# Kernel optimization log

Hardware: AMD Instinct MI355X
Metric: run time of the kernel (lower is better)

The kernel has to match this reference:

```python
import jax, jax.numpy as jnp
import numpy as np

NUM_CONTROL_POINTS = 4
# Standard Catmull-Rom spline basis (rows map [1, t, t^2, t^3] monomials to control points)
CATMULL_ROM_BASIS = 0.5 * np.array(
    [[0.0, 2.0, 0.0, 0.0],
     [-1.0, 0.0, 1.0, 0.0],
     [2.0, -5.0, 4.0, -1.0],
     [-1.0, 3.0, -3.0, 1.0]], dtype=np.float32)

BATCH, IN_F, OUT_F = 1024, 512, 512


def setup_inputs() -> dict:
    key = jax.random.key(0)
    k1, k2, k3, k4 = jax.random.split(key, 4)
    inp = jax.random.normal(k1, (BATCH, IN_F), dtype=jnp.float32)
    # phase spans [0, 2*pi) so both spline segments (mask = phase < 1.5*pi) are exercised
    phase = jax.random.uniform(k2, (BATCH,), dtype=jnp.float32) * (2.0 * jnp.pi)
    bound = 1.0 / np.sqrt(IN_F)
    weights = jax.random.uniform(k3, (NUM_CONTROL_POINTS, OUT_F, IN_F), dtype=jnp.float32,
                                 minval=-bound, maxval=bound)
    biases = jax.random.uniform(k4, (NUM_CONTROL_POINTS, OUT_F), dtype=jnp.float32,
                                minval=-bound, maxval=bound)
    return {"input": inp, "phase": phase, "weights": weights, "biases": biases}


def _spline_coeffs(phase):
    # Faithful to the original (including its overwrite bug): tt = [1, t^2, t^3, 0]
    basis = jnp.asarray(CATMULL_ROM_BASIS, dtype=phase.dtype)
    t0 = phase / (1.5 * jnp.pi)
    t1 = (phase - 0.5 * jnp.pi) / (1.5 * jnp.pi)
    ones, zeros = jnp.ones_like(phase), jnp.zeros_like(phase)
    tt0 = jnp.stack([ones, t0 * t0, t0 ** 3, zeros], axis=1)  # (B,4)
    tt1 = jnp.stack([ones, t1 * t1, t1 ** 3, zeros], axis=1)  # (B,4)
    mask = (phase < 1.5 * jnp.pi)[:, None]
    # Selecting per-sample coefficients before the weight contraction is exactly
    # equivalent to where(mask, tt0@B@W, tt1@B@W) since the map is linear in tt.
    return jnp.where(mask, tt0 @ basis, tt1 @ basis)  # (B,4) control-point coeffs


def reference(input, phase, weights, biases):
    c = _spline_coeffs(phase)                       # (B,4)
    # Fused form: apply the 4 shared control-point linear layers, then blend,
    # avoiding the (B,out,in) per-sample weight tensor. Same math as
    # (tt@B@W).reshape(B,out,in) @ input[:,:,None] + b.
    y4 = jnp.einsum('bi,coi->bco', input, weights)  # (B,4,out)
    out = jnp.einsum('bc,bco->bo', c, y4) + c @ biases  # (B,out)
    return out
```

## Files before the change

kernel.cpp:

```cpp
#include <hip/hip_runtime.h>


#define BATCH 1024
#define IN_F  512
#define OUT_F 512

constexpr int BM = 32;
constexpr int BO = 64;
constexpr int BK = 32;
constexpr int KITERS = IN_F / BK;
constexpr int A_ELEMS = BM * BK;
constexpr int TILE_ELEMS = (BM + 4 * BO) * BK;
constexpr int NVEC = TILE_ELEMS / 8;

typedef unsigned short u16;
typedef u16    u16x8  __attribute__((ext_vector_type(8)));
typedef __bf16 bf16x8 __attribute__((ext_vector_type(8)));
typedef float  f32x4  __attribute__((ext_vector_type(4)));

__device__ __forceinline__ u16 f2bits(float f) {
  union { float f; unsigned int u; } v; v.f = f;
  unsigned int u = v.u;
  unsigned int r = u + 0x7fffu + ((u >> 16) & 1u);
  return (u16)(r >> 16);
}

__global__ __launch_bounds__(256)
void PhaseLinear_kernel(const float* __restrict__ inp, const float* __restrict__ ph,
                        const float* __restrict__ wts, const float* __restrict__ bia,
                        float* __restrict__ outp) {
  __shared__ alignas(16) u16 sT[2][TILE_ELEMS];
  __shared__ float sCoef[BM][4];

  const int tid = threadIdx.x;
  const int wv  = tid >> 6;
  const int l   = tid & 63;
  const int o0  = blockIdx.x * BO;
  const int b0  = blockIdx.y * BM;

  if (tid < BM) {
    const float PI = 3.14159265358979323846f;
    float p  = ph[b0 + tid];
    float t  = (p < 1.5f * PI) ? (p / (1.5f * PI)) : ((p - 0.5f * PI) / (1.5f * PI));
    float t2 = t * t, t3 = t2 * t;
    sCoef[tid][0] = t3 - 0.5f * t2;
    sCoef[tid][1] = 1.0f - 2.5f * t3;
    sCoef[tid][2] = 0.5f * t2 + 2.0f * t3;
    sCoef[tid][3] = -0.5f * t3;
  }

  const int nv = (tid < NVEC - 1024) ? 5 : 4;
  const float* src[5];
  int loff[5];
#pragma unroll
  for (int j = 0; j < 5; ++j) {
    int v = tid + j * 256;
    if (v >= NVEC) { src[j] = inp; loff[j] = 0; continue; }
    int e = v * 8;
    loff[j] = e;
    if (e < A_ELEMS) {
      int row = e >> 5, col = e & 31;
      src[j] = inp + (size_t)(b0 + row) * IN_F + col;
    } else {
      int ep = e - A_ELEMS;
      int r = ep >> 5, col = ep & 31;
      int c = r >> 6, oo = r & 63;
      src[j] = wts + ((size_t)c * OUT_F + o0 + oo) * IN_F + col;
    }
  }

  f32x4 regs[5][2];
#pragma unroll
  for (int j = 0; j < 5; ++j)
    if (j < nv) {
      regs[j][0] = *(const f32x4*)(src[j]);
      regs[j][1] = *(const f32x4*)(src[j] + 4);
    }

  f32x4 acc[2][4];
#pragma unroll
  for (int m = 0; m < 2; ++m)
#pragma unroll
    for (int c = 0; c < 4; ++c) acc[m][c] = (f32x4){0.f, 0.f, 0.f, 0.f};

  const int q = l >> 4;
  const int n = l & 15;

  for (int kk = 0; kk < KITERS; ++kk) {
    const int bsel = kk & 1;
    u16* buf = &sT[bsel][0];
#pragma unroll
    for (int j = 0; j < 5; ++j)
      if (j < nv) {
        u16x8 pk;
#pragma unroll
        for (int x = 0; x < 4; ++x) {
          pk[x]     = f2bits(regs[j][0][x]);
          pk[x + 4] = f2bits(regs[j][1][x]);
        }
        *(u16x8*)(buf + loff[j]) = pk;
      }
    if (kk + 1 < KITERS) {
#pragma unroll
      for (int j = 0; j < 5; ++j)
        if (j < nv) {
          regs[j][0] = *(const f32x4*)(src[j] + (kk + 1) * BK);
          regs[j][1] = *(const f32x4*)(src[j] + (kk + 1) * BK + 4);
        }
    }
    __syncthreads();
    const u16* pA = buf;
    const u16* pW = buf + A_ELEMS;
    bf16x8 a0 = *(const bf16x8*)(pA + (n)      * BK + q * 8);
    bf16x8 a1 = *(const bf16x8*)(pA + (n + 16) * BK + q * 8);
#pragma unroll
    for (int c = 0; c < 4; ++c) {
      bf16x8 wf = *(const bf16x8*)(pW + (c * 64 + wv * 16 + n) * BK + q * 8);
      acc[0][c] = __builtin_amdgcn_mfma_f32_16x16x32_bf16(a0, wf, acc[0][c], 0, 0, 0);
      acc[1][c] = __builtin_amdgcn_mfma_f32_16x16x32_bf16(a1, wf, acc[1][c], 0, 0, 0);
    }
  }

  const int o = o0 + wv * 16 + n;
  float bs[4];
#pragma unroll
  for (int c = 0; c < 4; ++c) bs[c] = bia[c * OUT_F + o];

#pragma unroll
  for (int mf = 0; mf < 2; ++mf) {
#pragma unroll
    for (int r = 0; r < 4; ++r) {
      const int bl = mf * 16 + q * 4 + r;
      float v = 0.f;
#pragma unroll
      for (int c = 0; c < 4; ++c)
        v += sCoef[bl][c] * (acc[mf][c][r] + bs[c]);
      outp[(size_t)(b0 + bl) * OUT_F + o] = v;
    }
  }
}

extern "C" void kernel_launch(void* const* d_in, const int* in_sizes, int n_in,
                              void* d_out, int out_size, void* d_ws, size_t ws_size,
                              hipStream_t stream) {
  const float* inp = (const float*)d_in[0];
  const float* ph  = (const float*)d_in[1];
  const float* wts = (const float*)d_in[2];
  const float* bia = (const float*)d_in[3];
  float* outp = (float*)d_out;

  dim3 grid(OUT_F / BO, BATCH / BM);
  PhaseLinear_kernel<<<grid, 256, 0, stream>>>(inp, ph, wts, bia, outp);
}
```

Before: 75.56 us.

## Load MFMA fragments directly from global memory, dropping the LDS staging

Removes the shared-memory tile and its per-iteration barrier. Each lane now loads its own fp32 A and W fragments straight from global memory with 32-byte vector loads, converts them to bf16 in registers, and prefetches the next k-step into registers. The output tile shrinks to 32 columns with 128 threads per block, giving twice as many blocks. In exchange, the A rows are re-read by every wave and every block with no LDS reuse, so it relies on L2 and L1 to absorb the duplicate traffic.

Result: slower. 84.39 us (+11.7%).

```diff
diff --git a/kernel.cpp b/kernel.cpp
--- a/kernel.cpp
+++ b/kernel.cpp
@@ -6,30 +6,26 @@
 #define OUT_F 512
 
 constexpr int BM = 32;
-constexpr int BO = 64;
+constexpr int BO = 32;
 constexpr int BK = 32;
 constexpr int KITERS = IN_F / BK;
-constexpr int A_ELEMS = BM * BK;
-constexpr int TILE_ELEMS = (BM + 4 * BO) * BK;
-constexpr int NVEC = TILE_ELEMS / 8;
 
 typedef unsigned short u16;
-typedef u16    u16x8  __attribute__((ext_vector_type(8)));
 typedef __bf16 bf16x8 __attribute__((ext_vector_type(8)));
 typedef float  f32x4  __attribute__((ext_vector_type(4)));
+typedef float  f32x8  __attribute__((ext_vector_type(8)));
 
-__device__ __forceinline__ u16 f2bits(float f) {
-  union { float f; unsigned int u; } v; v.f = f;
-  unsigned int u = v.u;
-  unsigned int r = u + 0x7fffu + ((u >> 16) & 1u);
-  return (u16)(r >> 16);
+__device__ __forceinline__ bf16x8 cvt8(f32x8 v) {
+  bf16x8 r;
+#pragma unroll
+  for (int i = 0; i < 8; ++i) r[i] = (__bf16)v[i];
+  return r;
 }
 
-__global__ __launch_bounds__(256)
+__global__ __launch_bounds__(128)
 void PhaseLinear_kernel(const float* __restrict__ inp, const float* __restrict__ ph,
                         const float* __restrict__ wts, const float* __restrict__ bia,
                         float* __restrict__ outp) {
-  __shared__ alignas(16) u16 sT[2][TILE_ELEMS];
   __shared__ float sCoef[BM][4];
 
   const int tid = threadIdx.x;
@@ -48,34 +44,17 @@
     sCoef[tid][2] = 0.5f * t2 + 2.0f * t3;
     sCoef[tid][3] = -0.5f * t3;
   }
+  __syncthreads();
 
-  const int nv = (tid < NVEC - 1024) ? 5 : 4;
-  const float* src[5];
-  int loff[5];
+  const int n = l & 15;
+  const int q = l >> 4;
+
+  const float* pa0 = inp + (size_t)(b0 + n) * IN_F + q * 8;
+  const float* pa1 = pa0 + (size_t)16 * IN_F;
+  const float* pw[4];
 #pragma unroll
-  for (int j = 0; j < 5; ++j) {
-    int v = tid + j * 256;
-    if (v >= NVEC) { src[j] = inp; loff[j] = 0; continue; }
-    int e = v * 8;
-    loff[j] = e;
-    if (e < A_ELEMS) {
-      int row = e >> 5, col = e & 31;
-      src[j] = inp + (size_t)(b0 + row) * IN_F + col;
-    } else {
-      int ep = e - A_ELEMS;
-      int r = ep >> 5, col = ep & 31;
-      int c = r >> 6, oo = r & 63;
-      src[j] = wts + ((size_t)c * OUT_F + o0 + oo) * IN_F + col;
-    }
-  }
-
-  f32x4 regs[5][2];
-#pragma unroll
-  for (int j = 0; j < 5; ++j)
-    if (j < nv) {
-      regs[j][0] = *(const f32x4*)(src[j]);
-      regs[j][1] = *(const f32x4*)(src[j] + 4);
-    }
+  for (int c = 0; c < 4; ++c)
+    pw[c] = wts + ((size_t)c * OUT_F + o0 + wv * 16 + n) * IN_F + q * 8;
 
   f32x4 acc[2][4];
 #pragma unroll
@@ -83,42 +62,32 @@
 #pragma unroll
     for (int c = 0; c < 4; ++c) acc[m][c] = (f32x4){0.f, 0.f, 0.f, 0.f};
 
-  const int q = l >> 4;
-  const int n = l & 15;
+  f32x8 cur[6];
+  cur[0] = *(const f32x8*)(pa0);
+  cur[1] = *(const f32x8*)(pa1);
+#pragma unroll
+  for (int c = 0; c < 4; ++c) cur[2 + c] = *(const f32x8*)(pw[c]);
 
+#pragma unroll
   for (int kk = 0; kk < KITERS; ++kk) {
-    const int bsel = kk & 1;
-    u16* buf = &sT[bsel][0];
+    f32x8 nxt[6];
+    if (kk + 1 < KITERS) {
+      const int off = (kk + 1) * BK;
+      nxt[0] = *(const f32x8*)(pa0 + off);
+      nxt[1] = *(const f32x8*)(pa1 + off);
 #pragma unroll
-    for (int j = 0; j < 5; ++j)
-      if (j < nv) {
-        u16x8 pk;
-#pragma unroll
-        for (int x = 0; x < 4; ++x) {
-          pk[x]     = f2bits(regs[j][0][x]);
-          pk[x + 4] = f2bits(regs[j][1][x]);
-        }
-        *(u16x8*)(buf + loff[j]) = pk;
-      }
-    if (kk + 1 < KITERS) {
-#pragma unroll
-      for (int j = 0; j < 5; ++j)
-        if (j < nv) {
-          regs[j][0] = *(const f32x4*)(src[j] + (kk + 1) * BK);
-          regs[j][1] = *(const f32x4*)(src[j] + (kk + 1) * BK + 4);
-        }
+      for (int c = 0; c < 4; ++c) nxt[2 + c] = *(const f32x8*)(pw[c] + off);
     }
-    __syncthreads();
-    const u16* pA = buf;
-    const u16* pW = buf + A_ELEMS;
-    bf16x8 a0 = *(const bf16x8*)(pA + (n)      * BK + q * 8);
-    bf16x8 a1 = *(const bf16x8*)(pA + (n + 16) * BK + q * 8);
+    bf16x8 a0 = cvt8(cur[0]);
+    bf16x8 a1 = cvt8(cur[1]);
 #pragma unroll
     for (int c = 0; c < 4; ++c) {
-      bf16x8 wf = *(const bf16x8*)(pW + (c * 64 + wv * 16 + n) * BK + q * 8);
+      bf16x8 wf = cvt8(cur[2 + c]);
       acc[0][c] = __builtin_amdgcn_mfma_f32_16x16x32_bf16(a0, wf, acc[0][c], 0, 0, 0);
       acc[1][c] = __builtin_amdgcn_mfma_f32_16x16x32_bf16(a1, wf, acc[1][c], 0, 0, 0);
     }
+#pragma unroll
+    for (int j = 0; j < 6; ++j) cur[j] = nxt[j];
   }
 
   const int o = o0 + wv * 16 + n;
@@ -150,5 +119,5 @@
   float* outp = (float*)d_out;
 
   dim3 grid(OUT_F / BO, BATCH / BM);
-  PhaseLinear_kernel<<<grid, 256, 0, stream>>>(inp, ph, wts, bia, outp);
+  PhaseLinear_kernel<<<grid, 128, 0, stream>>>(inp, ph, wts, bia, outp);
 }
```
